# Performance work log

Measured on AMD Instinct MI355X. Metric: run time of the kernel, lower is better.

Reference implementation:

```python
import jax, jax.numpy as jnp
import numpy as np

N, DEG = 50000, 16
E = N * DEG
F_IN, HID, F_OUT, IJ = 128, 128, 128, 16


def _mlp2(x, W1, b1, W2, b2, tanh_out):
    y = jnp.tanh(x @ W1 + b1) @ W2 + b2
    return jnp.tanh(y) if tanh_out else y


def setup_inputs() -> dict:
    key = jax.random.key(0)
    ks = jax.random.split(key, 16)
    p = lambda k, sh: jax.random.normal(k, sh, dtype=jnp.float32) * 0.05
    inp = {
        "h": jax.random.normal(ks[0], (N, F_IN), dtype=jnp.float32),
        "x": jax.random.normal(ks[1], (N, 3), dtype=jnp.float32),
        "velocidade": jax.random.normal(ks[2], (N, 3), dtype=jnp.float32),
        "atributos_arestas": jax.random.normal(ks[3], (E, IJ), dtype=jnp.float32),
        "rows": jnp.repeat(jnp.arange(N, dtype=jnp.int32), DEG),
        "cols": jax.random.randint(ks[4], (E,), 0, N, dtype=jnp.int32),
        # phi_e: Linear(2F+1+IJ, HID), Tanh, Linear(HID, HID), Tanh
        "We1": p(ks[5], (2 * F_IN + 1 + IJ, HID)), "be1": jnp.zeros(HID, jnp.float32),
        "We2": p(ks[6], (HID, HID)), "be2": jnp.zeros(HID, jnp.float32),
        # phi_x: Linear(HID, HID), Tanh, Linear(HID, 1), Tanh
        "Wx1": p(ks[7], (HID, HID)), "bx1": jnp.zeros(HID, jnp.float32),
        "Wx2": p(ks[8], (HID, 1)), "bx2": jnp.zeros(1, jnp.float32),
        # phi_h: Linear(HID+1, HID), Tanh, Linear(HID, F_OUT)
        "Wh1": p(ks[9], (HID + 1, HID)), "bh1": jnp.zeros(HID, jnp.float32),
        "Wh2": p(ks[10], (HID, F_OUT)), "bh2": jnp.zeros(F_OUT, jnp.float32),
        # phi_v: Linear(F_IN, HID), Tanh, Linear(HID, 1)
        "Wv1": p(ks[11], (F_IN, HID)), "bv1": jnp.zeros(HID, jnp.float32),
        "Wv2": p(ks[12], (HID, 1)), "bv2": jnp.zeros(1, jnp.float32),
    }
    return inp


def reference(h, x, velocidade, atributos_arestas, rows, cols,
              We1, be1, We2, be2, Wx1, bx1, Wx2, bx2,
              Wh1, bh1, Wh2, bh2, Wv1, bv1, Wv2, bv2):
    n = h.shape[0]
    diff = x[rows] - x[cols]                              # [E, 3]
    dif_radial = jnp.sum(diff * diff, axis=1, keepdims=True)  # [E, 1]
    attrs = jnp.concatenate([h[rows], h[cols], dif_radial, atributos_arestas], axis=1)
    m_ij = _mlp2(attrs, We1, be1, We2, be2, tanh_out=True)    # [E, HID]
    phi_x = _mlp2(m_ij, Wx1, bx1, Wx2, bx2, tanh_out=True)    # [E, 1]
    phi_v = _mlp2(h, Wv1, bv1, Wv2, bv2, tanh_out=False)      # [N, 1]

    counts = jax.ops.segment_sum(jnp.ones_like(rows, dtype=diff.dtype), rows, num_segments=n)

    # media_segmentada: for edge (i=rows, j=cols): acc[i] += sum_over_features(edge_tensor[j])
    # (NOTE: indexes the EDGE tensor by the column NODE id j, faithful to source)
    ex = diff * phi_x                                     # [E, 3]
    vals = jnp.sum(ex[cols], axis=1)                      # [E]
    media = jax.ops.segment_sum(vals, rows, num_segments=n)
    media = jnp.where(counts > 0, media / counts, 0.0)[:, None]  # [N, 1]

    velocidade_new = velocidade * phi_v + media           # [N, 3]
    x_new = x + velocidade_new

    # soma_segmentada on m_ij with same quirky indexing
    m_vals = jnp.sum(m_ij[cols], axis=1)                  # [E]
    m_i = jax.ops.segment_sum(m_vals, rows, num_segments=n)[:, None]  # [N, 1]

    h_new = _mlp2(jnp.concatenate([h, m_i], axis=1), Wh1, bh1, Wh2, bh2, tanh_out=False)
    return h_new, x_new, velocidade_new
```

## Files before the change

### kernel.cpp

```cpp
#include <hip/hip_runtime.h>
#include <hip/hip_bf16.h>

#define NN      50000
#define DEG     16
#define FDIM    128
#define BM      64
#define ASTR    296
#define OSTR    136
#define OFF_WE1 0
#define OFF_WE2 36864
#define OFF_WX1 53248
#define OFF_WV1 69632
#define OFF_WH1 86016
#define OFF_WH2 102400
#define WS_SHORTS 118784

typedef short v8s  __attribute__((ext_vector_type(8)));
typedef short v4sh __attribute__((ext_vector_type(4)));
typedef short v2sh __attribute__((ext_vector_type(2)));
typedef float v4f  __attribute__((ext_vector_type(4)));

__device__ __forceinline__ float fast_tanh(float xv) {
    float ax = fabsf(xv);
    float e2 = __expf(2.0f * ax);
    float r  = 1.0f - 2.0f / (e2 + 1.0f);
    return copysignf(r, xv);
}

__device__ __forceinline__ short f2bf(float f) {
    union { float f; unsigned u; } a; a.f = f;
    unsigned r = a.u + 0x7fffu + ((a.u >> 16) & 1u);
    return (short)(unsigned short)(r >> 16);
}
__device__ __forceinline__ float bf2f(short s) {
    union { unsigned u; float f; } a; a.u = ((unsigned)(unsigned short)s) << 16;
    return a.f;
}

template<int KSTEPS, int KPAD>
__device__ __forceinline__ void load_B(const short* __restrict__ Wt, int l, int w,
                                       v8s B[KSTEPS][2])
{
    const int lm = l & 15, lk = l >> 4;
    const short* b0 = Wt + (size_t)(w * 32 + lm) * KPAD + lk * 8;
#pragma unroll
    for (int ks = 0; ks < KSTEPS; ++ks) {
        B[ks][0] = *(const v8s*)(b0 + ks * 32);
        B[ks][1] = *(const v8s*)(b0 + 16 * KPAD + ks * 32);
    }
}

__device__ __forceinline__ void acc_zero(v4f acc[4][2]) {
    v4f z = {0.f, 0.f, 0.f, 0.f};
#pragma unroll
    for (int mt = 0; mt < 4; ++mt) { acc[mt][0] = z; acc[mt][1] = z; }
}

template<int KSTEPS, int ASTRIDE>
__device__ __forceinline__ void mfma_acc(const short* A, const v8s B[KSTEPS][2],
                                         int l, v4f acc[4][2])
{
    const int lm = l & 15, lk = l >> 4;
    const short* ap = A + lm * ASTRIDE + lk * 8;
#pragma unroll
    for (int ks = 0; ks < KSTEPS; ++ks) {
        v8s a[4];
#pragma unroll
        for (int mt = 0; mt < 4; ++mt)
            a[mt] = *(const v8s*)(ap + mt * 16 * ASTRIDE + ks * 32);
#pragma unroll
        for (int mt = 0; mt < 4; ++mt) {
            acc[mt][0] = __builtin_amdgcn_mfma_f32_16x16x32_bf16(a[mt], B[ks][0], acc[mt][0], 0, 0, 0);
            acc[mt][1] = __builtin_amdgcn_mfma_f32_16x16x32_bf16(a[mt], B[ks][1], acc[mt][1], 0, 0, 0);
        }
    }
}

__device__ __forceinline__ void epi_to_lds(v4f acc[4][2], short* O,
                                           const float* __restrict__ b, int l, int w)
{
    const int rl = (l >> 4) * 4, cl = l & 15;
#pragma unroll
    for (int nt = 0; nt < 2; ++nt) {
        const int col = w * 32 + nt * 16 + cl;
        const float bias = b[col];
#pragma unroll
        for (int mt = 0; mt < 4; ++mt)
#pragma unroll
            for (int r = 0; r < 4; ++r)
                O[(mt * 16 + rl + r) * OSTR + col] = f2bf(fast_tanh(acc[mt][nt][r] + bias));
    }
}

__global__ __launch_bounds__(256) void prep_weights(
    const float* __restrict__ We1, const float* __restrict__ We2,
    const float* __restrict__ Wx1, const float* __restrict__ Wv1,
    const float* __restrict__ Wh1, const float* __restrict__ Wh2,
    short* __restrict__ wbuf)
{
    int idx = blockIdx.x * 256 + threadIdx.x;
    if (idx < 128 * 288) {
        int c = idx / 288, k = idx % 288;
        wbuf[OFF_WE1 + idx] = (k < 273) ? f2bf(We1[k * FDIM + c]) : (short)0;
        return;
    }
    idx -= 128 * 288;
    if (idx < 5 * 16384) {
        int layer = idx / 16384, r = idx % 16384;
        int c = r / 128, k = r % 128;
        const float* W = (layer == 0) ? We2 : (layer == 1) ? Wx1 :
                         (layer == 2) ? Wv1 : (layer == 3) ? Wh1 : Wh2;
        wbuf[OFF_WE2 + layer * 16384 + c * 128 + k] = f2bf(W[k * FDIM + c]);
    }
}

__global__ __launch_bounds__(256, 2) void edge_kernel(
    const float* __restrict__ h, const float* __restrict__ x,
    const float* __restrict__ ea, const int* __restrict__ cols,
    const short* __restrict__ wbuf,
    const float* __restrict__ be1, const float* __restrict__ be2,
    const float* __restrict__ bx1,
    const float* __restrict__ Wx2, const float* __restrict__ bx2,
    float* __restrict__ msum, float* __restrict__ exsum)
{
    __shared__ __align__(16) short bigbuf[BM * ASTR];
    __shared__ __align__(16) short buf1[BM * OSTR];
    __shared__ float sdiff[BM];

    short* attrs = bigbuf;
    short* buf2  = bigbuf;

    const int tid = threadIdx.x;
    const int e0  = blockIdx.x * BM;
    const int l   = tid & 63, w = tid >> 6;

    v8s B1[9][2];
    load_B<9, 288>(wbuf + OFF_WE1, l, w, B1);

    {
        const int el = tid >> 2, q = tid & 3;
        int ec = e0 + el; if (ec >= NN) ec = NN - 1;
        const int i = ec >> 4;
        const int j = cols[ec];
        const float4* hi4 = (const float4*)(h + (size_t)i * FDIM) + q * 8;
        const float4* hj4 = (const float4*)(h + (size_t)j * FDIM) + q * 8;
        short* arow = attrs + el * ASTR;
#pragma unroll
        for (int t = 0; t < 8; ++t) {
            float4 v = hi4[t];
            v4sh s = { f2bf(v.x), f2bf(v.y), f2bf(v.z), f2bf(v.w) };
            *(v4sh*)(arow + q * 32 + t * 4) = s;
            float4 u = hj4[t];
            v4sh s2 = { f2bf(u.x), f2bf(u.y), f2bf(u.z), f2bf(u.w) };
            *(v4sh*)(arow + 128 + q * 32 + t * 4) = s2;
        }
        if (q == 0) {
#pragma unroll
            for (int t = 0; t < 16; ++t)
                arow[257 + t] = f2bf(ea[(size_t)ec * 16 + t]);
        }
        if (q == 1) {
            float dx = x[i * 3 + 0] - x[j * 3 + 0];
            float dy = x[i * 3 + 1] - x[j * 3 + 1];
            float dz = x[i * 3 + 2] - x[j * 3 + 2];
            arow[256] = f2bf(dx * dx + dy * dy + dz * dz);
            sdiff[el] = dx + dy + dz;
        }
        if (q == 2) {
#pragma unroll
            for (int t = 0; t < 15; ++t) arow[273 + t] = 0;
        }
    }
    __syncthreads();

    v4f acc[4][2];
    acc_zero(acc);
    mfma_acc<9, ASTR>(attrs, B1, l, acc);
    v8s B2[4][2];
    load_B<4, 128>(wbuf + OFF_WE2, l, w, B2);
    epi_to_lds(acc, buf1, be1, l, w);
    __syncthreads();

    acc_zero(acc);
    mfma_acc<4, OSTR>(buf1, B2, l, acc);
    v8s B3[4][2];
    load_B<4, 128>(wbuf + OFF_WX1, l, w, B3);
    epi_to_lds(acc, buf2, be2, l, w);
    __syncthreads();

#pragma unroll
    for (int e = 0; e < 16; ++e) {
        int row = w * 16 + e;
        v2sh p = *(const v2sh*)(buf2 + row * OSTR + 2 * l);
        float s = bf2f(p.x) + bf2f(p.y);
#pragma unroll
        for (int m = 32; m >= 1; m >>= 1) s += __shfl_xor(s, m, 64);
        if (l == 0) {
            int eg = e0 + row;
            if (eg < NN) msum[eg] = s;
        }
    }

    acc_zero(acc);
    mfma_acc<4, OSTR>(buf2, B3, l, acc);
    epi_to_lds(acc, buf1, bx1, l, w);
    __syncthreads();

    {
        const float wx0 = Wx2[2 * l], wx1 = Wx2[2 * l + 1];
        const float bxx = bx2[0];
#pragma unroll
        for (int e = 0; e < 16; ++e) {
            int row = w * 16 + e;
            v2sh p = *(const v2sh*)(buf1 + row * OSTR + 2 * l);
            float s = bf2f(p.x) * wx0 + bf2f(p.y) * wx1;
#pragma unroll
            for (int m = 32; m >= 1; m >>= 1) s += __shfl_xor(s, m, 64);
            if (l == 0) {
                int eg = e0 + row;
                if (eg < NN) exsum[eg] = fast_tanh(s + bxx) * sdiff[row];
            }
        }
    }
}

__global__ __launch_bounds__(256, 3) void node_kernel(
    const float* __restrict__ h, const float* __restrict__ x,
    const float* __restrict__ vel, const int* __restrict__ cols,
    const short* __restrict__ wbuf,
    const float* __restrict__ bv1, const float* __restrict__ Wv2,
    const float* __restrict__ bv2,
    const float* __restrict__ bh1, const float* __restrict__ Wh1f,
    const float* __restrict__ bh2,
    const float* __restrict__ msum, const float* __restrict__ exsum,
    float* __restrict__ out_h, float* __restrict__ out_x, float* __restrict__ out_v)
{
    __shared__ __align__(16) short hn[BM * OSTR];
    __shared__ __align__(16) short buf1[BM * OSTR];
    __shared__ float mi[BM], media[BM], phiv[BM];

    const int tid = threadIdx.x;
    const int n0  = blockIdx.x * BM;
    const int l   = tid & 63, w = tid >> 6;

    v8s B1[4][2], B2[4][2];
    load_B<4, 128>(wbuf + OFF_WV1, l, w, B1);
    load_B<4, 128>(wbuf + OFF_WH1, l, w, B2);

    {
        const int el = tid >> 2, q = tid & 3;
        int nc = n0 + el; if (nc >= NN) nc = NN - 1;
        const float4* hr = (const float4*)(h + (size_t)nc * FDIM) + q * 8;
        short* arow = hn + el * OSTR;
#pragma unroll
        for (int t = 0; t < 8; ++t) {
            float4 v = hr[t];
            v4sh s = { f2bf(v.x), f2bf(v.y), f2bf(v.z), f2bf(v.w) };
            *(v4sh*)(arow + q * 32 + t * 4) = s;
        }
    }
    {
#pragma unroll
        for (int r = 0; r < 4; ++r) {
            int idx = tid + r * 256;
            int nl = idx >> 4, kk = idx & 15;
            int nc = n0 + nl; if (nc >= NN) nc = NN - 1;
            int c = cols[(size_t)nc * DEG + kk];
            float ms = msum[c];
            float ex = exsum[c];
#pragma unroll
            for (int m = 8; m >= 1; m >>= 1) {
                ms += __shfl_xor(ms, m, 64);
                ex += __shfl_xor(ex, m, 64);
            }
            if (kk == 0) { mi[nl] = ms; media[nl] = ex * (1.0f / 16.0f); }
        }
    }
    __syncthreads();

    v4f acc[4][2];
    acc_zero(acc);
    mfma_acc<4, OSTR>(hn, B1, l, acc);
    v8s B3[4][2];
    load_B<4, 128>(wbuf + OFF_WH2, l, w, B3);
    epi_to_lds(acc, buf1, bv1, l, w);
    __syncthreads();

    {
        const float wv0 = Wv2[2 * l], wv1 = Wv2[2 * l + 1];
        const float bvv = bv2[0];
#pragma unroll
        for (int e = 0; e < 16; ++e) {
            int row = w * 16 + e;
            v2sh p = *(const v2sh*)(buf1 + row * OSTR + 2 * l);
            float s = bf2f(p.x) * wv0 + bf2f(p.y) * wv1;
#pragma unroll
            for (int m = 32; m >= 1; m >>= 1) s += __shfl_xor(s, m, 64);
            if (l == 0) phiv[row] = s + bvv;
        }
    }
    __syncthreads();

    acc_zero(acc);
    mfma_acc<4, OSTR>(hn, B2, l, acc);
    {
        const int rl = (l >> 4) * 4, cl = l & 15;
        const float* w128 = Wh1f + (size_t)FDIM * FDIM;
#pragma unroll
        for (int nt = 0; nt < 2; ++nt) {
            const int col = w * 32 + nt * 16 + cl;
            const float bias = bh1[col], wr = w128[col];
#pragma unroll
            for (int mt = 0; mt < 4; ++mt)
#pragma unroll
                for (int r = 0; r < 4; ++r) {
                    int row = mt * 16 + rl + r;
                    buf1[row * OSTR + col] =
                        f2bf(fast_tanh(acc[mt][nt][r] + bias + mi[row] * wr));
                }
        }
    }
    __syncthreads();

    acc_zero(acc);
    mfma_acc<4, OSTR>(buf1, B3, l, acc);
    {
        const int rl = (l >> 4) * 4, cl = l & 15;
#pragma unroll
        for (int nt = 0; nt < 2; ++nt) {
            const int col = w * 32 + nt * 16 + cl;
            const float bias = bh2[col];
#pragma unroll
            for (int mt = 0; mt < 4; ++mt)
#pragma unroll
                for (int r = 0; r < 4; ++r) {
                    int rg = n0 + mt * 16 + rl + r;
                    if (rg < NN) out_h[(size_t)rg * FDIM + col] = acc[mt][nt][r] + bias;
                }
        }
    }

    if (tid < BM * 3) {
        int nl = tid / 3, d = tid % 3;
        int n = n0 + nl;
        if (n < NN) {
            float vv = vel[(size_t)n * 3 + d] * phiv[nl] + media[nl];
            out_v[(size_t)n * 3 + d] = vv;
            out_x[(size_t)n * 3 + d] = x[(size_t)n * 3 + d] + vv;
        }
    }
}

extern "C" void kernel_launch(void* const* d_in, const int* in_sizes, int n_in,
                              void* d_out, int out_size, void* d_ws, size_t ws_size,
                              hipStream_t stream)
{
    (void)in_sizes; (void)n_in; (void)out_size; (void)ws_size;
    const float* h    = (const float*)d_in[0];
    const float* x    = (const float*)d_in[1];
    const float* vel  = (const float*)d_in[2];
    const float* ea   = (const float*)d_in[3];
    const int*   cols = (const int*)d_in[5];
    const float* We1 = (const float*)d_in[6];  const float* be1 = (const float*)d_in[7];
    const float* We2 = (const float*)d_in[8];  const float* be2 = (const float*)d_in[9];
    const float* Wx1 = (const float*)d_in[10]; const float* bx1 = (const float*)d_in[11];
    const float* Wx2 = (const float*)d_in[12]; const float* bx2 = (const float*)d_in[13];
    const float* Wh1 = (const float*)d_in[14]; const float* bh1 = (const float*)d_in[15];
    const float* Wh2 = (const float*)d_in[16]; const float* bh2 = (const float*)d_in[17];
    const float* Wv1 = (const float*)d_in[18]; const float* bv1 = (const float*)d_in[19];
    const float* Wv2 = (const float*)d_in[20]; const float* bv2 = (const float*)d_in[21];

    short* wbuf  = (short*)d_ws;
    float* msum  = (float*)((char*)d_ws + WS_SHORTS * sizeof(short));
    float* exsum = msum + NN;
    float* out_h = (float*)d_out;
    float* out_x = out_h + (size_t)NN * FDIM;
    float* out_v = out_x + (size_t)NN * 3;

    dim3 block(256);
    prep_weights<<<dim3((WS_SHORTS + 255) / 256), block, 0, stream>>>(
        We1, We2, Wx1, Wv1, Wh1, Wh2, wbuf);
    dim3 grid((NN + BM - 1) / BM);
    edge_kernel<<<grid, block, 0, stream>>>(h, x, ea, cols, wbuf,
                                            be1, be2, bx1, Wx2, bx2, msum, exsum);
    node_kernel<<<grid, block, 0, stream>>>(h, x, vel, cols, wbuf,
                                            bv1, Wv2, bv2, bh1, Wh1, bh2,
                                            msum, exsum, out_h, out_x, out_v);
}
```

Before: 236.3 us.

## Halve row tile, fuse row reductions into MFMA epilogues, stream B weights

Cuts the edge and node row tile from 64 to 32, which doubles the block count and shrinks LDS and register use per block. It also removes the 2-per-SIMD launch-bound hints. The msum, phi_x and phi_v row reductions now happen in registers inside the MFMA epilogues through 16-lane shuffles and per-wave partials, instead of writing bf16 to LDS and reducing again. For the 128-wide layers the B weight fragments are loaded from global inside the K loop rather than held in registers, trading extra weight reloads per block for lower register pressure and more occupancy. The extra weight loads and more blocks could offset the gains.

```diff
diff --git a/kernel.cpp b/kernel.cpp
--- a/kernel.cpp
+++ b/kernel.cpp
@@ -4,7 +4,7 @@
 #define NN      50000
 #define DEG     16
 #define FDIM    128
-#define BM      64
+#define BM      32
 #define ASTR    296
 #define OSTR    136
 #define OFF_WE1 0
@@ -17,7 +17,6 @@
 
 typedef short v8s  __attribute__((ext_vector_type(8)));
 typedef short v4sh __attribute__((ext_vector_type(4)));
-typedef short v2sh __attribute__((ext_vector_type(2)));
 typedef float v4f  __attribute__((ext_vector_type(4)));
 
 __device__ __forceinline__ float fast_tanh(float xv) {
@@ -32,10 +31,6 @@
     unsigned r = a.u + 0x7fffu + ((a.u >> 16) & 1u);
     return (short)(unsigned short)(r >> 16);
 }
-__device__ __forceinline__ float bf2f(short s) {
-    union { unsigned u; float f; } a; a.u = ((unsigned)(unsigned short)s) << 16;
-    return a.f;
-}
 
 template<int KSTEPS, int KPAD>
 __device__ __forceinline__ void load_B(const short* __restrict__ Wt, int l, int w,
@@ -50,34 +45,50 @@
     }
 }
 
-__device__ __forceinline__ void acc_zero(v4f acc[4][2]) {
+__device__ __forceinline__ void acc_zero(v4f acc[2][2]) {
     v4f z = {0.f, 0.f, 0.f, 0.f};
-#pragma unroll
-    for (int mt = 0; mt < 4; ++mt) { acc[mt][0] = z; acc[mt][1] = z; }
+    acc[0][0] = z; acc[0][1] = z; acc[1][0] = z; acc[1][1] = z;
 }
 
 template<int KSTEPS, int ASTRIDE>
-__device__ __forceinline__ void mfma_acc(const short* A, const v8s B[KSTEPS][2],
-                                         int l, v4f acc[4][2])
+__device__ __forceinline__ void mfma_regB(const short* A, const v8s B[KSTEPS][2],
+                                          int l, v4f acc[2][2])
 {
     const int lm = l & 15, lk = l >> 4;
     const short* ap = A + lm * ASTRIDE + lk * 8;
 #pragma unroll
     for (int ks = 0; ks < KSTEPS; ++ks) {
-        v8s a[4];
-#pragma unroll
-        for (int mt = 0; mt < 4; ++mt)
-            a[mt] = *(const v8s*)(ap + mt * 16 * ASTRIDE + ks * 32);
-#pragma unroll
-        for (int mt = 0; mt < 4; ++mt) {
-            acc[mt][0] = __builtin_amdgcn_mfma_f32_16x16x32_bf16(a[mt], B[ks][0], acc[mt][0], 0, 0, 0);
-            acc[mt][1] = __builtin_amdgcn_mfma_f32_16x16x32_bf16(a[mt], B[ks][1], acc[mt][1], 0, 0, 0);
-        }
-    }
-}
-
-__device__ __forceinline__ void epi_to_lds(v4f acc[4][2], short* O,
-                                           const float* __restrict__ b, int l, int w)
+        v8s a0 = *(const v8s*)(ap + ks * 32);
+        v8s a1 = *(const v8s*)(ap + 16 * ASTRIDE + ks * 32);
+        acc[0][0] = __builtin_amdgcn_mfma_f32_16x16x32_bf16(a0, B[ks][0], acc[0][0], 0, 0, 0);
+        acc[1][0] = __builtin_amdgcn_mfma_f32_16x16x32_bf16(a1, B[ks][0], acc[1][0], 0, 0, 0);
+        acc[0][1] = __builtin_amdgcn_mfma_f32_16x16x32_bf16(a0, B[ks][1], acc[0][1], 0, 0, 0);
+        acc[1][1] = __builtin_amdgcn_mfma_f32_16x16x32_bf16(a1, B[ks][1], acc[1][1], 0, 0, 0);
+    }
+}
+
+template<int KSTEPS, int ASTRIDE>
+__device__ __forceinline__ void mfma_ldB(const short* A, const short* __restrict__ Wt,
+                                         int l, int w, v4f acc[2][2])
+{
+    const int lm = l & 15, lk = l >> 4;
+    const short* ap = A + lm * ASTRIDE + lk * 8;
+    const short* b0 = Wt + (size_t)(w * 32 + lm) * 128 + lk * 8;
+#pragma unroll
+    for (int ks = 0; ks < KSTEPS; ++ks) {
+        v8s a0 = *(const v8s*)(ap + ks * 32);
+        v8s a1 = *(const v8s*)(ap + 16 * ASTRIDE + ks * 32);
+        v8s bb0 = *(const v8s*)(b0 + ks * 32);
+        v8s bb1 = *(const v8s*)(b0 + 16 * 128 + ks * 32);
+        acc[0][0] = __builtin_amdgcn_mfma_f32_16x16x32_bf16(a0, bb0, acc[0][0], 0, 0, 0);
+        acc[1][0] = __builtin_amdgcn_mfma_f32_16x16x32_bf16(a1, bb0, acc[1][0], 0, 0, 0);
+        acc[0][1] = __builtin_amdgcn_mfma_f32_16x16x32_bf16(a0, bb1, acc[0][1], 0, 0, 0);
+        acc[1][1] = __builtin_amdgcn_mfma_f32_16x16x32_bf16(a1, bb1, acc[1][1], 0, 0, 0);
+    }
+}
+
+__device__ __forceinline__ void epi_tanh_lds(v4f acc[2][2], short* O,
+                                             const float* __restrict__ b, int l, int w)
 {
     const int rl = (l >> 4) * 4, cl = l & 15;
 #pragma unroll
@@ -85,11 +96,28 @@
         const int col = w * 32 + nt * 16 + cl;
         const float bias = b[col];
 #pragma unroll
-        for (int mt = 0; mt < 4; ++mt)
+        for (int mt = 0; mt < 2; ++mt)
 #pragma unroll
             for (int r = 0; r < 4; ++r)
                 O[(mt * 16 + rl + r) * OSTR + col] = f2bf(fast_tanh(acc[mt][nt][r] + bias));
     }
+}
+
+__device__ __forceinline__ void row_part_store(float part[2][4], float* part_out,
+                                               int l, int w)
+{
+    const int rl = (l >> 4) * 4;
+#pragma unroll
+    for (int mt = 0; mt < 2; ++mt)
+#pragma unroll
+        for (int r = 0; r < 4; ++r) {
+            float s = part[mt][r];
+            s += __shfl_xor(s, 1, 64);
+            s += __shfl_xor(s, 2, 64);
+            s += __shfl_xor(s, 4, 64);
+            s += __shfl_xor(s, 8, 64);
+            if ((l & 15) == 0) part_out[w * BM + mt * 16 + rl + r] = s;
+        }
 }
 
 __global__ __launch_bounds__(256) void prep_weights(
@@ -114,7 +142,7 @@
     }
 }
 
-__global__ __launch_bounds__(256, 2) void edge_kernel(
+__global__ __launch_bounds__(256) void edge_kernel(
     const float* __restrict__ h, const float* __restrict__ x,
     const float* __restrict__ ea, const int* __restrict__ cols,
     const short* __restrict__ wbuf,
@@ -126,6 +154,8 @@
     __shared__ __align__(16) short bigbuf[BM * ASTR];
     __shared__ __align__(16) short buf1[BM * OSTR];
     __shared__ float sdiff[BM];
+    __shared__ float part_m[4 * BM];
+    __shared__ float part_p[4 * BM];
 
     short* attrs = bigbuf;
     short* buf2  = bigbuf;
@@ -138,93 +168,101 @@
     load_B<9, 288>(wbuf + OFF_WE1, l, w, B1);
 
     {
-        const int el = tid >> 2, q = tid & 3;
+        const int el = tid >> 3, q = tid & 7;
         int ec = e0 + el; if (ec >= NN) ec = NN - 1;
         const int i = ec >> 4;
         const int j = cols[ec];
-        const float4* hi4 = (const float4*)(h + (size_t)i * FDIM) + q * 8;
-        const float4* hj4 = (const float4*)(h + (size_t)j * FDIM) + q * 8;
+        const float4* hi4 = (const float4*)(h + (size_t)i * FDIM);
+        const float4* hj4 = (const float4*)(h + (size_t)j * FDIM);
         short* arow = attrs + el * ASTR;
 #pragma unroll
-        for (int t = 0; t < 8; ++t) {
-            float4 v = hi4[t];
+        for (int t = 0; t < 4; ++t) {
+            float4 v = hi4[q * 4 + t];
             v4sh s = { f2bf(v.x), f2bf(v.y), f2bf(v.z), f2bf(v.w) };
-            *(v4sh*)(arow + q * 32 + t * 4) = s;
-            float4 u = hj4[t];
+            *(v4sh*)(arow + q * 16 + t * 4) = s;
+            float4 u = hj4[q * 4 + t];
             v4sh s2 = { f2bf(u.x), f2bf(u.y), f2bf(u.z), f2bf(u.w) };
-            *(v4sh*)(arow + 128 + q * 32 + t * 4) = s2;
-        }
-        if (q == 0) {
-#pragma unroll
-            for (int t = 0; t < 16; ++t)
-                arow[257 + t] = f2bf(ea[(size_t)ec * 16 + t]);
-        }
-        if (q == 1) {
+            *(v4sh*)(arow + 128 + q * 16 + t * 4) = s2;
+        }
+        if (q < 2) {
+#pragma unroll
+            for (int t = 0; t < 8; ++t)
+                arow[257 + q * 8 + t] = f2bf(ea[(size_t)ec * 16 + q * 8 + t]);
+        }
+        if (q == 2) {
             float dx = x[i * 3 + 0] - x[j * 3 + 0];
             float dy = x[i * 3 + 1] - x[j * 3 + 1];
             float dz = x[i * 3 + 2] - x[j * 3 + 2];
             arow[256] = f2bf(dx * dx + dy * dy + dz * dz);
             sdiff[el] = dx + dy + dz;
         }
-        if (q == 2) {
+        if (q == 3) {
 #pragma unroll
             for (int t = 0; t < 15; ++t) arow[273 + t] = 0;
         }
     }
     __syncthreads();
 
-    v4f acc[4][2];
-    acc_zero(acc);
-    mfma_acc<9, ASTR>(attrs, B1, l, acc);
-    v8s B2[4][2];
-    load_B<4, 128>(wbuf + OFF_WE2, l, w, B2);
-    epi_to_lds(acc, buf1, be1, l, w);
-    __syncthreads();
-
-    acc_zero(acc);
-    mfma_acc<4, OSTR>(buf1, B2, l, acc);
-    v8s B3[4][2];
-    load_B<4, 128>(wbuf + OFF_WX1, l, w, B3);
-    epi_to_lds(acc, buf2, be2, l, w);
-    __syncthreads();
-
-#pragma unroll
-    for (int e = 0; e < 16; ++e) {
-        int row = w * 16 + e;
-        v2sh p = *(const v2sh*)(buf2 + row * OSTR + 2 * l);
-        float s = bf2f(p.x) + bf2f(p.y);
-#pragma unroll
-        for (int m = 32; m >= 1; m >>= 1) s += __shfl_xor(s, m, 64);
-        if (l == 0) {
-            int eg = e0 + row;
-            if (eg < NN) msum[eg] = s;
-        }
-    }
-
-    acc_zero(acc);
-    mfma_acc<4, OSTR>(buf2, B3, l, acc);
-    epi_to_lds(acc, buf1, bx1, l, w);
-    __syncthreads();
-
-    {
-        const float wx0 = Wx2[2 * l], wx1 = Wx2[2 * l + 1];
-        const float bxx = bx2[0];
-#pragma unroll
-        for (int e = 0; e < 16; ++e) {
-            int row = w * 16 + e;
-            v2sh p = *(const v2sh*)(buf1 + row * OSTR + 2 * l);
-            float s = bf2f(p.x) * wx0 + bf2f(p.y) * wx1;
-#pragma unroll
-            for (int m = 32; m >= 1; m >>= 1) s += __shfl_xor(s, m, 64);
-            if (l == 0) {
-                int eg = e0 + row;
-                if (eg < NN) exsum[eg] = fast_tanh(s + bxx) * sdiff[row];
-            }
-        }
-    }
-}
-
-__global__ __launch_bounds__(256, 3) void node_kernel(
+    v4f acc[2][2];
+    acc_zero(acc);
+    mfma_regB<9, ASTR>(attrs, B1, l, acc);
+    epi_tanh_lds(acc, buf1, be1, l, w);
+    __syncthreads();
+
+    acc_zero(acc);
+    mfma_ldB<4, OSTR>(buf1, wbuf + OFF_WE2, l, w, acc);
+    {
+        const int rl = (l >> 4) * 4, cl = l & 15;
+        float part[2][4] = {{0,0,0,0},{0,0,0,0}};
+#pragma unroll
+        for (int nt = 0; nt < 2; ++nt) {
+            const int col = w * 32 + nt * 16 + cl;
+            const float bias = be2[col];
+#pragma unroll
+            for (int mt = 0; mt < 2; ++mt)
+#pragma unroll
+                for (int r = 0; r < 4; ++r) {
+                    float t = fast_tanh(acc[mt][nt][r] + bias);
+                    buf2[(mt * 16 + rl + r) * OSTR + col] = f2bf(t);
+                    part[mt][r] += t;
+                }
+        }
+        row_part_store(part, part_m, l, w);
+    }
+    __syncthreads();
+
+    acc_zero(acc);
+    mfma_ldB<4, OSTR>(buf2, wbuf + OFF_WX1, l, w, acc);
+    {
+        const int cl = l & 15;
+        float part[2][4] = {{0,0,0,0},{0,0,0,0}};
+#pragma unroll
+        for (int nt = 0; nt < 2; ++nt) {
+            const int col = w * 32 + nt * 16 + cl;
+            const float bias = bx1[col];
+            const float wx = Wx2[col];
+#pragma unroll
+            for (int mt = 0; mt < 2; ++mt)
+#pragma unroll
+                for (int r = 0; r < 4; ++r)
+                    part[mt][r] += fast_tanh(acc[mt][nt][r] + bias) * wx;
+        }
+        row_part_store(part, part_p, l, w);
+    }
+    __syncthreads();
+
+    if (tid < BM) {
+        int row = tid, eg = e0 + row;
+        float ms = part_m[row] + part_m[BM + row] + part_m[2 * BM + row] + part_m[3 * BM + row];
+        if (eg < NN) msum[eg] = ms;
+    } else if (tid < 2 * BM) {
+        int row = tid - BM, eg = e0 + row;
+        float ps = part_p[row] + part_p[BM + row] + part_p[2 * BM + row] + part_p[3 * BM + row];
+        if (eg < NN) exsum[eg] = fast_tanh(ps + bx2[0]) * sdiff[row];
+    }
+}
+
+__global__ __launch_bounds__(256) void node_kernel(
     const float* __restrict__ h, const float* __restrict__ x,
     const float* __restrict__ vel, const int* __restrict__ cols,
     const short* __restrict__ wbuf,
@@ -237,31 +275,28 @@
 {
     __shared__ __align__(16) short hn[BM * OSTR];
     __shared__ __align__(16) short buf1[BM * OSTR];
-    __shared__ float mi[BM], media[BM], phiv[BM];
+    __shared__ float mi[BM], media[BM];
+    __shared__ float part_v[4 * BM];
 
     const int tid = threadIdx.x;
     const int n0  = blockIdx.x * BM;
     const int l   = tid & 63, w = tid >> 6;
 
-    v8s B1[4][2], B2[4][2];
-    load_B<4, 128>(wbuf + OFF_WV1, l, w, B1);
-    load_B<4, 128>(wbuf + OFF_WH1, l, w, B2);
-
-    {
-        const int el = tid >> 2, q = tid & 3;
+    {
+        const int el = tid >> 3, q = tid & 7;
         int nc = n0 + el; if (nc >= NN) nc = NN - 1;
-        const float4* hr = (const float4*)(h + (size_t)nc * FDIM) + q * 8;
+        const float4* hr = (const float4*)(h + (size_t)nc * FDIM);
         short* arow = hn + el * OSTR;
 #pragma unroll
-        for (int t = 0; t < 8; ++t) {
-            float4 v = hr[t];
+        for (int t = 0; t < 4; ++t) {
+            float4 v = hr[q * 4 + t];
             v4sh s = { f2bf(v.x), f2bf(v.y), f2bf(v.z), f2bf(v.w) };
-            *(v4sh*)(arow + q * 32 + t * 4) = s;
-        }
-    }
-    {
-#pragma unroll
-        for (int r = 0; r < 4; ++r) {
+            *(v4sh*)(arow + q * 16 + t * 4) = s;
+        }
+    }
+    {
+#pragma unroll
+        for (int r = 0; r < 2; ++r) {
             int idx = tid + r * 256;
             int nl = idx >> 4, kk = idx & 15;
             int nc = n0 + nl; if (nc >= NN) nc = NN - 1;
@@ -278,31 +313,27 @@
     }
     __syncthreads();
 
-    v4f acc[4][2];
-    acc_zero(acc);
-    mfma_acc<4, OSTR>(hn, B1, l, acc);
-    v8s B3[4][2];
-    load_B<4, 128>(wbuf + OFF_WH2, l, w, B3);
-    epi_to_lds(acc, buf1, bv1, l, w);
-    __syncthreads();
-
-    {
-        const float wv0 = Wv2[2 * l], wv1 = Wv2[2 * l + 1];
-        const float bvv = bv2[0];
-#pragma unroll
-        for (int e = 0; e < 16; ++e) {
-            int row = w * 16 + e;
-            v2sh p = *(const v2sh*)(buf1 + row * OSTR + 2 * l);
-            float s = bf2f(p.x) * wv0 + bf2f(p.y) * wv1;
-#pragma unroll
-            for (int m = 32; m >= 1; m >>= 1) s += __shfl_xor(s, m, 64);
-            if (l == 0) phiv[row] = s + bvv;
-        }
-    }
-    __syncthreads();
-
-    acc_zero(acc);
-    mfma_acc<4, OSTR>(hn, B2, l, acc);
+    v4f acc[2][2];
+    acc_zero(acc);
+    mfma_ldB<4, OSTR>(hn, wbuf + OFF_WV1, l, w, acc);
+    {
+        const int cl = l & 15;
+        float part[2][4] = {{0,0,0,0},{0,0,0,0}};
+#pragma unroll
+        for (int nt = 0; nt < 2; ++nt) {
+            const int col = w * 32 + nt * 16 + cl;
+            const float bias = bv1[col];
+            const float wv = Wv2[col];
+#pragma unroll
+            for (int mt = 0; mt < 2; ++mt)
+#pragma unroll
+                for (int r = 0; r < 4; ++r)
+                    part[mt][r] += fast_tanh(acc[mt][nt][r] + bias) * wv;
+        }
+        row_part_store(part, part_v, l, w);
+    }
+    acc_zero(acc);
+    mfma_ldB<4, OSTR>(hn, wbuf + OFF_WH1, l, w, acc);
     {
         const int rl = (l >> 4) * 4, cl = l & 15;
         const float* w128 = Wh1f + (size_t)FDIM * FDIM;
@@ -311,7 +342,7 @@
             const int col = w * 32 + nt * 16 + cl;
             const float bias = bh1[col], wr = w128[col];
 #pragma unroll
-            for (int mt = 0; mt < 4; ++mt)
+            for (int mt = 0; mt < 2; ++mt)
 #pragma unroll
                 for (int r = 0; r < 4; ++r) {
                     int row = mt * 16 + rl + r;
@@ -323,7 +354,7 @@
     __syncthreads();
 
     acc_zero(acc);
-    mfma_acc<4, OSTR>(buf1, B3, l, acc);
+    mfma_ldB<4, OSTR>(buf1, wbuf + OFF_WH2, l, w, acc);
     {
         const int rl = (l >> 4) * 4, cl = l & 15;
 #pragma unroll
@@ -331,7 +362,7 @@
             const int col = w * 32 + nt * 16 + cl;
             const float bias = bh2[col];
 #pragma unroll
-            for (int mt = 0; mt < 4; ++mt)
+            for (int mt = 0; mt < 2; ++mt)
 #pragma unroll
                 for (int r = 0; r < 4; ++r) {
                     int rg = n0 + mt * 16 + rl + r;
@@ -344,7 +375,9 @@
         int nl = tid / 3, d = tid % 3;
         int n = n0 + nl;
         if (n < NN) {
-            float vv = vel[(size_t)n * 3 + d] * phiv[nl] + media[nl];
+            float pv = bv2[0] + part_v[nl] + part_v[BM + nl]
+                     + part_v[2 * BM + nl] + part_v[3 * BM + nl];
+            float vv = vel[(size_t)n * 3 + d] * pv + media[nl];
             out_v[(size_t)n * 3 + d] = vv;
             out_x[(size_t)n * 3 + d] = x[(size_t)n * 3 + d] + vv;
         }
```

Result: faster. 218.4 us (-7.6%).

## Restructure edge and node kernels to per-wave 16-row tiles without block syncs

Applied to the files above, without the earlier changes.

Each wave now independently handles 16 edges or nodes. The A fragments are loaded straight from global memory into registers, B weights are streamed from global for every MFMA, and a small per-wave LDS tile is used only to transpose between layers. This removes the block-wide __syncthreads, the large shared attrs buffer and the register-cached B fragments, and it raises the occupancy hint to 3 blocks. In exchange, weights are re-read from global or cache by every wave instead of once per block, and reductions are done with row-wise shuffles.

```diff
diff --git a/kernel.cpp b/kernel.cpp
--- a/kernel.cpp
+++ b/kernel.cpp
@@ -4,8 +4,7 @@
 #define NN      50000
 #define DEG     16
 #define FDIM    128
-#define BM      64
-#define ASTR    296
+#define BPW     16
 #define OSTR    136
 #define OFF_WE1 0
 #define OFF_WE2 36864
@@ -16,8 +15,6 @@
 #define WS_SHORTS 118784
 
 typedef short v8s  __attribute__((ext_vector_type(8)));
-typedef short v4sh __attribute__((ext_vector_type(4)));
-typedef short v2sh __attribute__((ext_vector_type(2)));
 typedef float v4f  __attribute__((ext_vector_type(4)));
 
 __device__ __forceinline__ float fast_tanh(float xv) {
@@ -32,64 +29,11 @@
     unsigned r = a.u + 0x7fffu + ((a.u >> 16) & 1u);
     return (short)(unsigned short)(r >> 16);
 }
-__device__ __forceinline__ float bf2f(short s) {
-    union { unsigned u; float f; } a; a.u = ((unsigned)(unsigned short)s) << 16;
-    return a.f;
-}
-
-template<int KSTEPS, int KPAD>
-__device__ __forceinline__ void load_B(const short* __restrict__ Wt, int l, int w,
-                                       v8s B[KSTEPS][2])
-{
-    const int lm = l & 15, lk = l >> 4;
-    const short* b0 = Wt + (size_t)(w * 32 + lm) * KPAD + lk * 8;
-#pragma unroll
-    for (int ks = 0; ks < KSTEPS; ++ks) {
-        B[ks][0] = *(const v8s*)(b0 + ks * 32);
-        B[ks][1] = *(const v8s*)(b0 + 16 * KPAD + ks * 32);
-    }
-}
-
-__device__ __forceinline__ void acc_zero(v4f acc[4][2]) {
-    v4f z = {0.f, 0.f, 0.f, 0.f};
-#pragma unroll
-    for (int mt = 0; mt < 4; ++mt) { acc[mt][0] = z; acc[mt][1] = z; }
-}
-
-template<int KSTEPS, int ASTRIDE>
-__device__ __forceinline__ void mfma_acc(const short* A, const v8s B[KSTEPS][2],
-                                         int l, v4f acc[4][2])
-{
-    const int lm = l & 15, lk = l >> 4;
-    const short* ap = A + lm * ASTRIDE + lk * 8;
-#pragma unroll
-    for (int ks = 0; ks < KSTEPS; ++ks) {
-        v8s a[4];
-#pragma unroll
-        for (int mt = 0; mt < 4; ++mt)
-            a[mt] = *(const v8s*)(ap + mt * 16 * ASTRIDE + ks * 32);
-#pragma unroll
-        for (int mt = 0; mt < 4; ++mt) {
-            acc[mt][0] = __builtin_amdgcn_mfma_f32_16x16x32_bf16(a[mt], B[ks][0], acc[mt][0], 0, 0, 0);
-            acc[mt][1] = __builtin_amdgcn_mfma_f32_16x16x32_bf16(a[mt], B[ks][1], acc[mt][1], 0, 0, 0);
-        }
-    }
-}
-
-__device__ __forceinline__ void epi_to_lds(v4f acc[4][2], short* O,
-                                           const float* __restrict__ b, int l, int w)
-{
-    const int rl = (l >> 4) * 4, cl = l & 15;
-#pragma unroll
-    for (int nt = 0; nt < 2; ++nt) {
-        const int col = w * 32 + nt * 16 + cl;
-        const float bias = b[col];
-#pragma unroll
-        for (int mt = 0; mt < 4; ++mt)
-#pragma unroll
-            for (int r = 0; r < 4; ++r)
-                O[(mt * 16 + rl + r) * OSTR + col] = f2bf(fast_tanh(acc[mt][nt][r] + bias));
-    }
+
+__device__ __forceinline__ v8s pack8(float4 a, float4 b) {
+    v8s s = { f2bf(a.x), f2bf(a.y), f2bf(a.z), f2bf(a.w),
+              f2bf(b.x), f2bf(b.y), f2bf(b.z), f2bf(b.w) };
+    return s;
 }
 
 __global__ __launch_bounds__(256) void prep_weights(
@@ -114,7 +58,57 @@
     }
 }
 
-__global__ __launch_bounds__(256, 2) void edge_kernel(
+template<int KSTEPS>
+__device__ __forceinline__ void mfma_16rows(const v8s* af, const short* __restrict__ Wt,
+                                            int lm, int lk, v4f acc[8])
+{
+#pragma unroll
+    for (int ft = 0; ft < 8; ++ft) {
+        const short* bp = Wt + (size_t)(ft * 16 + lm) * (KSTEPS * 32) + lk * 8;
+#pragma unroll
+        for (int kc = 0; kc < KSTEPS; ++kc) {
+            v8s b = *(const v8s*)(bp + kc * 32);
+            acc[ft] = __builtin_amdgcn_mfma_f32_16x16x32_bf16(af[kc], b, acc[ft], 0, 0, 0);
+        }
+    }
+}
+
+__device__ __forceinline__ void acc_zero8(v4f acc[8]) {
+    v4f z = {0.f, 0.f, 0.f, 0.f};
+#pragma unroll
+    for (int ft = 0; ft < 8; ++ft) acc[ft] = z;
+}
+
+__device__ __forceinline__ void epi_transpose(v4f acc[8], short* tb,
+                                              const float* __restrict__ b,
+                                              int lm, int lk)
+{
+#pragma unroll
+    for (int ft = 0; ft < 8; ++ft) {
+        const int col = ft * 16 + lm;
+        const float bias = b[col];
+#pragma unroll
+        for (int r = 0; r < 4; ++r)
+            tb[(lk * 4 + r) * OSTR + col] = f2bf(fast_tanh(acc[ft][r] + bias));
+    }
+}
+
+__device__ __forceinline__ void load_af_lds(const short* tb, int lm, int lk, v8s af[4])
+{
+#pragma unroll
+    for (int kc = 0; kc < 4; ++kc)
+        af[kc] = *(const v8s*)(tb + lm * OSTR + kc * 32 + lk * 8);
+}
+
+__device__ __forceinline__ float red16(float s) {
+    s += __shfl_xor(s, 1, 64);
+    s += __shfl_xor(s, 2, 64);
+    s += __shfl_xor(s, 4, 64);
+    s += __shfl_xor(s, 8, 64);
+    return s;
+}
+
+__global__ __launch_bounds__(256, 3) void edge_kernel(
     const float* __restrict__ h, const float* __restrict__ x,
     const float* __restrict__ ea, const int* __restrict__ cols,
     const short* __restrict__ wbuf,
@@ -123,103 +117,106 @@
     const float* __restrict__ Wx2, const float* __restrict__ bx2,
     float* __restrict__ msum, float* __restrict__ exsum)
 {
-    __shared__ __align__(16) short bigbuf[BM * ASTR];
-    __shared__ __align__(16) short buf1[BM * OSTR];
-    __shared__ float sdiff[BM];
-
-    short* attrs = bigbuf;
-    short* buf2  = bigbuf;
+    __shared__ __align__(16) short tbuf[4][BPW * OSTR];
 
     const int tid = threadIdx.x;
-    const int e0  = blockIdx.x * BM;
     const int l   = tid & 63, w = tid >> 6;
-
-    v8s B1[9][2];
-    load_B<9, 288>(wbuf + OFF_WE1, l, w, B1);
-
-    {
-        const int el = tid >> 2, q = tid & 3;
-        int ec = e0 + el; if (ec >= NN) ec = NN - 1;
-        const int i = ec >> 4;
-        const int j = cols[ec];
-        const float4* hi4 = (const float4*)(h + (size_t)i * FDIM) + q * 8;
-        const float4* hj4 = (const float4*)(h + (size_t)j * FDIM) + q * 8;
-        short* arow = attrs + el * ASTR;
-#pragma unroll
-        for (int t = 0; t < 8; ++t) {
-            float4 v = hi4[t];
-            v4sh s = { f2bf(v.x), f2bf(v.y), f2bf(v.z), f2bf(v.w) };
-            *(v4sh*)(arow + q * 32 + t * 4) = s;
-            float4 u = hj4[t];
-            v4sh s2 = { f2bf(u.x), f2bf(u.y), f2bf(u.z), f2bf(u.w) };
-            *(v4sh*)(arow + 128 + q * 32 + t * 4) = s2;
-        }
-        if (q == 0) {
-#pragma unroll
-            for (int t = 0; t < 16; ++t)
-                arow[257 + t] = f2bf(ea[(size_t)ec * 16 + t]);
-        }
-        if (q == 1) {
-            float dx = x[i * 3 + 0] - x[j * 3 + 0];
-            float dy = x[i * 3 + 1] - x[j * 3 + 1];
-            float dz = x[i * 3 + 2] - x[j * 3 + 2];
-            arow[256] = f2bf(dx * dx + dy * dy + dz * dz);
-            sdiff[el] = dx + dy + dz;
-        }
-        if (q == 2) {
-#pragma unroll
-            for (int t = 0; t < 15; ++t) arow[273 + t] = 0;
-        }
-    }
-    __syncthreads();
-
-    v4f acc[4][2];
-    acc_zero(acc);
-    mfma_acc<9, ASTR>(attrs, B1, l, acc);
-    v8s B2[4][2];
-    load_B<4, 128>(wbuf + OFF_WE2, l, w, B2);
-    epi_to_lds(acc, buf1, be1, l, w);
-    __syncthreads();
-
-    acc_zero(acc);
-    mfma_acc<4, OSTR>(buf1, B2, l, acc);
-    v8s B3[4][2];
-    load_B<4, 128>(wbuf + OFF_WX1, l, w, B3);
-    epi_to_lds(acc, buf2, be2, l, w);
-    __syncthreads();
-
-#pragma unroll
-    for (int e = 0; e < 16; ++e) {
-        int row = w * 16 + e;
-        v2sh p = *(const v2sh*)(buf2 + row * OSTR + 2 * l);
-        float s = bf2f(p.x) + bf2f(p.y);
-#pragma unroll
-        for (int m = 32; m >= 1; m >>= 1) s += __shfl_xor(s, m, 64);
-        if (l == 0) {
-            int eg = e0 + row;
-            if (eg < NN) msum[eg] = s;
-        }
-    }
-
-    acc_zero(acc);
-    mfma_acc<4, OSTR>(buf2, B3, l, acc);
-    epi_to_lds(acc, buf1, bx1, l, w);
-    __syncthreads();
-
-    {
-        const float wx0 = Wx2[2 * l], wx1 = Wx2[2 * l + 1];
+    const int wv  = blockIdx.x * 4 + w;
+    const int e0  = wv * BPW;
+    if (e0 >= NN) return;
+    const int lm = l & 15, lk = l >> 4;
+    short* tb = &tbuf[w][0];
+
+    const int i  = e0 >> 4;
+    const int jj = cols[e0 + lm];
+
+    float dx = x[i * 3 + 0] - x[jj * 3 + 0];
+    float dy = x[i * 3 + 1] - x[jj * 3 + 1];
+    float dz = x[i * 3 + 2] - x[jj * 3 + 2];
+    const float dr    = dx * dx + dy * dy + dz * dz;
+    const float sdiff = dx + dy + dz;
+
+    v8s af[9];
+#pragma unroll
+    for (int kc = 0; kc < 4; ++kc) {
+        const float4* p = (const float4*)(h + (size_t)i * FDIM + kc * 32 + lk * 8);
+        af[kc] = pack8(p[0], p[1]);
+    }
+#pragma unroll
+    for (int kc = 0; kc < 4; ++kc) {
+        const float4* p = (const float4*)(h + (size_t)jj * FDIM + kc * 32 + lk * 8);
+        af[kc + 4] = pack8(p[0], p[1]);
+    }
+    {
+        const float* earow = ea + (size_t)(e0 + lm) * 16;
+        float4 ea0 = *(const float4*)(earow);
+        float4 ea1 = *(const float4*)(earow + 4);
+        float4 ea2 = *(const float4*)(earow + 8);
+        float4 ea3 = *(const float4*)(earow + 12);
+        v8s z = {0,0,0,0,0,0,0,0};
+        if (lk == 0) {
+            v8s s = { f2bf(dr), f2bf(ea0.x), f2bf(ea0.y), f2bf(ea0.z),
+                      f2bf(ea0.w), f2bf(ea1.x), f2bf(ea1.y), f2bf(ea1.z) };
+            af[8] = s;
+        } else if (lk == 1) {
+            v8s s = { f2bf(ea1.w), f2bf(ea2.x), f2bf(ea2.y), f2bf(ea2.z),
+                      f2bf(ea2.w), f2bf(ea3.x), f2bf(ea3.y), f2bf(ea3.z) };
+            af[8] = s;
+        } else if (lk == 2) {
+            v8s s = { f2bf(ea3.w), 0, 0, 0, 0, 0, 0, 0 };
+            af[8] = s;
+        } else af[8] = z;
+    }
+
+    v4f acc[8];
+    acc_zero8(acc);
+    mfma_16rows<9>(af, wbuf + OFF_WE1, lm, lk, acc);
+    epi_transpose(acc, tb, be1, lm, lk);
+
+    v8s am[4];
+    load_af_lds(tb, lm, lk, am);
+    acc_zero8(acc);
+    mfma_16rows<4>(am, wbuf + OFF_WE2, lm, lk, acc);
+    {
+        float p[4] = {0.f, 0.f, 0.f, 0.f};
+#pragma unroll
+        for (int ft = 0; ft < 8; ++ft) {
+            const int col = ft * 16 + lm;
+            const float bias = be2[col];
+#pragma unroll
+            for (int r = 0; r < 4; ++r) {
+                float t = fast_tanh(acc[ft][r] + bias);
+                tb[(lk * 4 + r) * OSTR + col] = f2bf(t);
+                p[r] += t;
+            }
+        }
+#pragma unroll
+        for (int r = 0; r < 4; ++r) {
+            float s = red16(p[r]);
+            if (lm == 0) msum[e0 + lk * 4 + r] = s;
+        }
+    }
+
+    load_af_lds(tb, lm, lk, am);
+    acc_zero8(acc);
+    mfma_16rows<4>(am, wbuf + OFF_WX1, lm, lk, acc);
+    {
+        float p[4] = {0.f, 0.f, 0.f, 0.f};
+#pragma unroll
+        for (int ft = 0; ft < 8; ++ft) {
+            const int col = ft * 16 + lm;
+            const float bias = bx1[col];
+            const float wx = Wx2[col];
+#pragma unroll
+            for (int r = 0; r < 4; ++r)
+                p[r] += fast_tanh(acc[ft][r] + bias) * wx;
+        }
         const float bxx = bx2[0];
 #pragma unroll
-        for (int e = 0; e < 16; ++e) {
-            int row = w * 16 + e;
-            v2sh p = *(const v2sh*)(buf1 + row * OSTR + 2 * l);
-            float s = bf2f(p.x) * wx0 + bf2f(p.y) * wx1;
-#pragma unroll
-            for (int m = 32; m >= 1; m >>= 1) s += __shfl_xor(s, m, 64);
-            if (l == 0) {
-                int eg = e0 + row;
-                if (eg < NN) exsum[eg] = fast_tanh(s + bxx) * sdiff[row];
-            }
+        for (int r = 0; r < 4; ++r) {
+            float s  = red16(p[r]);
+            float sd = __shfl(sdiff, lk * 4 + r, 64);
+            if (lm == 0) exsum[e0 + lk * 4 + r] = fast_tanh(s + bxx) * sd;
         }
     }
 }
@@ -235,118 +232,93 @@
     const float* __restrict__ msum, const float* __restrict__ exsum,
     float* __restrict__ out_h, float* __restrict__ out_x, float* __restrict__ out_v)
 {
-    __shared__ __align__(16) short hn[BM * OSTR];
-    __shared__ __align__(16) short buf1[BM * OSTR];
-    __shared__ float mi[BM], media[BM], phiv[BM];
+    __shared__ __align__(16) short tbuf[4][BPW * OSTR];
 
     const int tid = threadIdx.x;
-    const int n0  = blockIdx.x * BM;
     const int l   = tid & 63, w = tid >> 6;
-
-    v8s B1[4][2], B2[4][2];
-    load_B<4, 128>(wbuf + OFF_WV1, l, w, B1);
-    load_B<4, 128>(wbuf + OFF_WH1, l, w, B2);
-
-    {
-        const int el = tid >> 2, q = tid & 3;
-        int nc = n0 + el; if (nc >= NN) nc = NN - 1;
-        const float4* hr = (const float4*)(h + (size_t)nc * FDIM) + q * 8;
-        short* arow = hn + el * OSTR;
-#pragma unroll
-        for (int t = 0; t < 8; ++t) {
-            float4 v = hr[t];
-            v4sh s = { f2bf(v.x), f2bf(v.y), f2bf(v.z), f2bf(v.w) };
-            *(v4sh*)(arow + q * 32 + t * 4) = s;
-        }
-    }
-    {
-#pragma unroll
-        for (int r = 0; r < 4; ++r) {
-            int idx = tid + r * 256;
-            int nl = idx >> 4, kk = idx & 15;
-            int nc = n0 + nl; if (nc >= NN) nc = NN - 1;
-            int c = cols[(size_t)nc * DEG + kk];
-            float ms = msum[c];
-            float ex = exsum[c];
-#pragma unroll
-            for (int m = 8; m >= 1; m >>= 1) {
-                ms += __shfl_xor(ms, m, 64);
-                ex += __shfl_xor(ex, m, 64);
-            }
-            if (kk == 0) { mi[nl] = ms; media[nl] = ex * (1.0f / 16.0f); }
-        }
-    }
-    __syncthreads();
-
-    v4f acc[4][2];
-    acc_zero(acc);
-    mfma_acc<4, OSTR>(hn, B1, l, acc);
-    v8s B3[4][2];
-    load_B<4, 128>(wbuf + OFF_WH2, l, w, B3);
-    epi_to_lds(acc, buf1, bv1, l, w);
-    __syncthreads();
-
-    {
-        const float wv0 = Wv2[2 * l], wv1 = Wv2[2 * l + 1];
-        const float bvv = bv2[0];
-#pragma unroll
-        for (int e = 0; e < 16; ++e) {
-            int row = w * 16 + e;
-            v2sh p = *(const v2sh*)(buf1 + row * OSTR + 2 * l);
-            float s = bf2f(p.x) * wv0 + bf2f(p.y) * wv1;
-#pragma unroll
-            for (int m = 32; m >= 1; m >>= 1) s += __shfl_xor(s, m, 64);
-            if (l == 0) phiv[row] = s + bvv;
-        }
-    }
-    __syncthreads();
-
-    acc_zero(acc);
-    mfma_acc<4, OSTR>(hn, B2, l, acc);
-    {
-        const int rl = (l >> 4) * 4, cl = l & 15;
+    const int wv  = blockIdx.x * 4 + w;
+    const int n0  = wv * BPW;
+    if (n0 >= NN) return;
+    const int lm = l & 15, lk = l >> 4;
+    short* tb = &tbuf[w][0];
+
+    float ms = 0.f, ex = 0.f;
+#pragma unroll
+    for (int t = 0; t < 4; ++t) {
+        int c = cols[(size_t)(n0 + lm) * DEG + lk * 4 + t];
+        ms += msum[c];
+        ex += exsum[c];
+    }
+    ms += __shfl_xor(ms, 16, 64); ms += __shfl_xor(ms, 32, 64);
+    ex += __shfl_xor(ex, 16, 64); ex += __shfl_xor(ex, 32, 64);
+    const float media = ex * (1.0f / 16.0f);
+
+    v8s ah[4];
+#pragma unroll
+    for (int kc = 0; kc < 4; ++kc) {
+        const float4* p = (const float4*)(h + (size_t)(n0 + lm) * FDIM + kc * 32 + lk * 8);
+        ah[kc] = pack8(p[0], p[1]);
+    }
+
+    v4f acc[8];
+    acc_zero8(acc);
+    mfma_16rows<4>(ah, wbuf + OFF_WV1, lm, lk, acc);
+    float pv[4];
+    {
+        float p[4] = {0.f, 0.f, 0.f, 0.f};
+#pragma unroll
+        for (int ft = 0; ft < 8; ++ft) {
+            const int col = ft * 16 + lm;
+            const float bias = bv1[col];
+            const float wvv = Wv2[col];
+#pragma unroll
+            for (int r = 0; r < 4; ++r)
+                p[r] += fast_tanh(acc[ft][r] + bias) * wvv;
+        }
+#pragma unroll
+        for (int r = 0; r < 4; ++r) pv[r] = red16(p[r]);
+    }
+
+    acc_zero8(acc);
+    mfma_16rows<4>(ah, wbuf + OFF_WH1, lm, lk, acc);
+    {
+        float mi_r[4];
+#pragma unroll
+        for (int r = 0; r < 4; ++r) mi_r[r] = __shfl(ms, lk * 4 + r, 64);
         const float* w128 = Wh1f + (size_t)FDIM * FDIM;
 #pragma unroll
-        for (int nt = 0; nt < 2; ++nt) {
-            const int col = w * 32 + nt * 16 + cl;
+        for (int ft = 0; ft < 8; ++ft) {
+            const int col = ft * 16 + lm;
             const float bias = bh1[col], wr = w128[col];
 #pragma unroll
-            for (int mt = 0; mt < 4; ++mt)
-#pragma unroll
-                for (int r = 0; r < 4; ++r) {
-                    int row = mt * 16 + rl + r;
-                    buf1[row * OSTR + col] =
-                        f2bf(fast_tanh(acc[mt][nt][r] + bias + mi[row] * wr));
-                }
-        }
-    }
-    __syncthreads();
-
-    acc_zero(acc);
-    mfma_acc<4, OSTR>(buf1, B3, l, acc);
-    {
-        const int rl = (l >> 4) * 4, cl = l & 15;
-#pragma unroll
-        for (int nt = 0; nt < 2; ++nt) {
-            const int col = w * 32 + nt * 16 + cl;
-            const float bias = bh2[col];
-#pragma unroll
-            for (int mt = 0; mt < 4; ++mt)
-#pragma unroll
-                for (int r = 0; r < 4; ++r) {
-                    int rg = n0 + mt * 16 + rl + r;
-                    if (rg < NN) out_h[(size_t)rg * FDIM + col] = acc[mt][nt][r] + bias;
-                }
-        }
-    }
-
-    if (tid < BM * 3) {
-        int nl = tid / 3, d = tid % 3;
-        int n = n0 + nl;
-        if (n < NN) {
-            float vv = vel[(size_t)n * 3 + d] * phiv[nl] + media[nl];
-            out_v[(size_t)n * 3 + d] = vv;
-            out_x[(size_t)n * 3 + d] = x[(size_t)n * 3 + d] + vv;
+            for (int r = 0; r < 4; ++r)
+                tb[(lk * 4 + r) * OSTR + col] =
+                    f2bf(fast_tanh(acc[ft][r] + bias + mi_r[r] * wr));
+        }
+    }
+
+    v8s am[4];
+    load_af_lds(tb, lm, lk, am);
+    acc_zero8(acc);
+    mfma_16rows<4>(am, wbuf + OFF_WH2, lm, lk, acc);
+#pragma unroll
+    for (int ft = 0; ft < 8; ++ft) {
+        const int col = ft * 16 + lm;
+        const float bias = bh2[col];
+#pragma unroll
+        for (int r = 0; r < 4; ++r)
+            out_h[(size_t)(n0 + lk * 4 + r) * FDIM + col] = acc[ft][r] + bias;
+    }
+
+    const float bvv = bv2[0];
+#pragma unroll
+    for (int r = 0; r < 4; ++r) {
+        float media_r = __shfl(media, lk * 4 + r, 64);
+        if (lm < 3) {
+            int n = n0 + lk * 4 + r;
+            float vv = vel[(size_t)n * 3 + lm] * (pv[r] + bvv) + media_r;
+            out_v[(size_t)n * 3 + lm] = vv;
+            out_x[(size_t)n * 3 + lm] = x[(size_t)n * 3 + lm] + vv;
         }
     }
 }
@@ -380,7 +352,8 @@
     dim3 block(256);
     prep_weights<<<dim3((WS_SHORTS + 255) / 256), block, 0, stream>>>(
         We1, We2, Wx1, Wv1, Wh1, Wh2, wbuf);
-    dim3 grid((NN + BM - 1) / BM);
+    const int nwaves = (NN + BPW - 1) / BPW;
+    dim3 grid((nwaves + 3) / 4);
     edge_kernel<<<grid, block, 0, stream>>>(h, x, ea, cols, wbuf,
                                             be1, be2, bx1, Wx2, bx2, msum, exsum);
     node_kernel<<<grid, block, 0, stream>>>(h, x, vel, cols, wbuf,
```

Result: slower. 258.2 us (+9.3%).
